# Kernel tuning notes

Measured on AMD Instinct MI355X. Metric: run time of the kernel, lower is better.

## Reference

```python
import jax, jax.numpy as jnp
import numpy as np

N_DOCS = 2_000_000      # shape[0]: number of documents
N_TERMS = 30_000        # vocabulary size (number of CSC columns)
NNZ_PER_COL = 2_000     # posting-list length per term (uniform)
Q = 32                  # active terms in the sparse query
TOP_K = 10


def setup_inputs() -> dict:
    key = jax.random.key(0)
    k1, k2, k3, k4 = jax.random.split(key, 4)
    # Uniform-length CSC column pointers: ccol[t] = t * NNZ_PER_COL
    ccol = jnp.arange(N_TERMS + 1, dtype=jnp.int32) * NNZ_PER_COL
    nnz = N_TERMS * NNZ_PER_COL
    rindices = jax.random.randint(k1, (nnz,), 0, N_DOCS, dtype=jnp.int32)
    cvalues = jax.random.uniform(k2, (nnz,), dtype=jnp.float32)
    indices = jax.random.randint(k3, (1, Q), 0, N_TERMS, dtype=jnp.int32)
    values = jax.random.normal(k4, (1, Q), dtype=jnp.float32)
    return {"ccol": ccol, "rindices": rindices, "cvalues": cvalues,
            "indices": indices, "values": values,
            "n_docs": N_DOCS, "top_k": TOP_K}


def reference(ccol, rindices, cvalues, indices, values, n_docs, top_k):
    idx = indices.reshape(-1)   # [Q] query term ids
    w = values.reshape(-1)      # [Q] query term weights
    # Static max posting-list length (uniform CSC built in setup_inputs).
    L = rindices.shape[0] // (ccol.shape[0] - 1)
    starts = ccol[idx]                       # [Q]
    lens = ccol[idx + 1] - starts            # [Q]
    offs = jnp.arange(L, dtype=starts.dtype) # [L]
    mask = offs[None, :] < lens[:, None]     # [Q, L] valid entries (handles ragged lists)
    pos = jnp.where(mask, starts[:, None] + offs[None, :], 0)  # [Q, L]
    docs = rindices[pos]                                        # [Q, L] doc ids
    contrib = jnp.where(mask, cvalues[pos] * w[:, None], 0.0)   # [Q, L] scaled scores
    # Scatter-add over documents (equivalent to the per-term index_add_ loop).
    accumulated = jnp.zeros((n_docs,), jnp.float32).at[docs.reshape(-1)].add(
        contrib.reshape(-1))
    top_vals, top_idx = jax.lax.top_k(accumulated, top_k)
    return top_vals, top_idx
```

## Files before the change

### kernel.cpp

```cpp
#include <hip/hip_runtime.h>
#include <float.h>
#include <limits.h>


#define TOPK 10
#define BLK  256

__device__ __forceinline__ bool better(float va, int ia, float vb, int ib) {
    return (va > vb) || (va == vb && ia < ib);
}

__device__ __forceinline__ void topk_insert(float (&lv)[TOPK], int (&li)[TOPK],
                                            float v, int i) {
    if (!better(v, i, lv[TOPK - 1], li[TOPK - 1])) return;
#pragma unroll
    for (int k = TOPK - 1; k >= 1; --k) {
        bool ck  = better(v, i, lv[k],     li[k]);
        bool ck1 = better(v, i, lv[k - 1], li[k - 1]);
        float nv = ck ? (ck1 ? lv[k - 1] : v) : lv[k];
        int   ni = ck ? (ck1 ? li[k - 1] : i) : li[k];
        lv[k] = nv; li[k] = ni;
    }
    if (better(v, i, lv[0], li[0])) { lv[0] = v; li[0] = i; }
}

__device__ void block_topk_merge(float (&lv)[TOPK], int (&li)[TOPK],
                                 float* sv, int* si, int tid) {
#pragma unroll
    for (int k = 0; k < TOPK; ++k) { sv[tid * TOPK + k] = lv[k]; si[tid * TOPK + k] = li[k]; }
    for (int off = BLK / 2; off >= 1; off >>= 1) {
        __syncthreads();
        if (tid < off) {
            const int ba = tid * TOPK, bb = (tid + off) * TOPK;
            float mv[TOPK]; int mi[TOPK];
            int a = 0, b = 0;
#pragma unroll
            for (int k = 0; k < TOPK; ++k) {
                float va = sv[ba + a]; int ia = si[ba + a];
                float vb = sv[bb + b]; int ib = si[bb + b];
                bool ta = better(va, ia, vb, ib);
                mv[k] = ta ? va : vb;
                mi[k] = ta ? ia : ib;
                a += ta ? 1 : 0;
                b += ta ? 0 : 1;
            }
#pragma unroll
            for (int k = 0; k < TOPK; ++k) { sv[ba + k] = mv[k]; si[ba + k] = mi[k]; }
        }
    }
    __syncthreads();
}

__global__ void __launch_bounds__(BLK)
zero_touched(const int* __restrict__ ccol, const int* __restrict__ rindices,
             const int* __restrict__ qidx, float* __restrict__ score, int L) {
    const int q = blockIdx.y;
    const int l = blockIdx.x * BLK + threadIdx.x;
    const int term  = qidx[q];
    const int start = ccol[term];
    const int len   = ccol[term + 1] - start;
    if (l < len && l < L) score[rindices[start + l]] = 0.0f;
}

__global__ void __launch_bounds__(BLK)
scatter_add(const int* __restrict__ ccol, const int* __restrict__ rindices,
            const float* __restrict__ cvalues, const int* __restrict__ qidx,
            const float* __restrict__ qval, float* __restrict__ score, int L) {
    const int q = blockIdx.y;
    const int l = blockIdx.x * BLK + threadIdx.x;
    const int term  = qidx[q];
    const int start = ccol[term];
    const int len   = ccol[term + 1] - start;
    if (l < len && l < L) {
        const int pos = start + l;
        atomicAdd(&score[rindices[pos]], cvalues[pos] * qval[q]);
    }
}

__global__ void __launch_bounds__(BLK)
candidates_topk(const int* __restrict__ ccol, const int* __restrict__ rindices,
                const int* __restrict__ qidx, float* __restrict__ score,
                float* __restrict__ cand_v, int* __restrict__ cand_i, int L) {
    __shared__ float sv[BLK * TOPK];
    __shared__ int   si[BLK * TOPK];
    float lv[TOPK]; int li[TOPK];
#pragma unroll
    for (int k = 0; k < TOPK; ++k) { lv[k] = -FLT_MAX; li[k] = INT_MAX; }

    const int q = blockIdx.y;
    const int l = blockIdx.x * BLK + threadIdx.x;
    const int term  = qidx[q];
    const int start = ccol[term];
    const int len   = ccol[term + 1] - start;
    if (l < len && l < L) {
        const int doc = rindices[start + l];
        const float v = atomicExch(&score[doc], -FLT_MAX);
        if (v != -FLT_MAX) topk_insert(lv, li, v, doc);
    }
    block_topk_merge(lv, li, sv, si, threadIdx.x);
    if (threadIdx.x == 0) {
        const int bid = blockIdx.y * gridDim.x + blockIdx.x;
#pragma unroll
        for (int k = 0; k < TOPK; ++k) {
            cand_v[bid * TOPK + k] = sv[k];
            cand_i[bid * TOPK + k] = si[k];
        }
    }
}

__global__ void __launch_bounds__(BLK)
final_topk(const float* __restrict__ cand_v, const int* __restrict__ cand_i,
           int ncand, float* __restrict__ out) {
    __shared__ float sv[BLK * TOPK];
    __shared__ int   si[BLK * TOPK];
    float lv[TOPK]; int li[TOPK];
#pragma unroll
    for (int k = 0; k < TOPK; ++k) { lv[k] = -FLT_MAX; li[k] = INT_MAX; }
    for (int t = threadIdx.x; t < ncand; t += BLK)
        topk_insert(lv, li, cand_v[t], cand_i[t]);
    block_topk_merge(lv, li, sv, si, threadIdx.x);
    if (threadIdx.x == 0) {
#pragma unroll
        for (int k = 0; k < TOPK; ++k) {
            out[k]        = sv[k];
            out[TOPK + k] = (float)si[k];
        }
    }
}

extern "C" void kernel_launch(void* const* d_in, const int* in_sizes, int n_in,
                              void* d_out, int out_size, void* d_ws, size_t ws_size,
                              hipStream_t stream) {
    const int*   ccol     = (const int*)  d_in[0];
    const int*   rindices = (const int*)  d_in[1];
    const float* cvalues  = (const float*)d_in[2];
    const int*   qidx     = (const int*)  d_in[3];
    const float* qval     = (const float*)d_in[4];
    const int n_docs = 2000000;
    const int nterms = in_sizes[0] - 1;
    const int Q      = in_sizes[3];
    const int L      = in_sizes[1] / nterms;

    float* score  = (float*)d_ws;
    char*  p      = (char*)d_ws + (size_t)n_docs * sizeof(float);
    const int lb  = (L + BLK - 1) / BLK;
    const int nblocks = lb * Q;
    float* cand_v = (float*)p;
    int*   cand_i = (int*)(p + (size_t)nblocks * TOPK * sizeof(float));

    dim3 grid(lb, Q);
    zero_touched   <<<grid, BLK, 0, stream>>>(ccol, rindices, qidx, score, L);
    scatter_add    <<<grid, BLK, 0, stream>>>(ccol, rindices, cvalues, qidx, qval, score, L);
    candidates_topk<<<grid, BLK, 0, stream>>>(ccol, rindices, qidx, score, cand_v, cand_i, L);
    final_topk     <<<1,    BLK, 0, stream>>>(cand_v, cand_i, nblocks * TOPK, (float*)d_out);
}
```

Before: 400.5 us.

## Fuse retrieval kernels into one cooperative kernel with grid-wide syncs

Replaces the four launches (zero touched docs, scatter-add, candidate top-k, final top-k) with a single cooperative kernel that separates the phases with grid.sync(). Each thread keeps its doc id and scaled contribution in registers across phases, so posting-list entries are not reloaded. The aim is to remove inter-kernel launch gaps and redundant global loads. In exchange it pays for three grid-wide barriers, needs every block to be resident at once, and adds host-side occupancy and attribute queries, falling back to the old four-kernel path when a cooperative launch is not possible.

```diff
diff --git a/kernel.cpp b/kernel.cpp
--- a/kernel.cpp
+++ b/kernel.cpp
@@ -1,10 +1,13 @@
 #include <hip/hip_runtime.h>
+#include <hip/hip_cooperative_groups.h>
 #include <float.h>
 #include <limits.h>
 
 
 #define TOPK 10
 #define BLK  256
+
+namespace cg = cooperative_groups;
 
 __device__ __forceinline__ bool better(float va, int ia, float vb, int ib) {
     return (va > vb) || (va == vb && ia < ib);
@@ -51,6 +54,71 @@
     __syncthreads();
 }
 
+
+__global__ void __launch_bounds__(BLK, 1)
+fused_retrieval(const int* __restrict__ ccol, const int* __restrict__ rindices,
+                const float* __restrict__ cvalues, const int* __restrict__ qidx,
+                const float* __restrict__ qval, float* __restrict__ score,
+                float* __restrict__ cand_v, int* __restrict__ cand_i,
+                float* __restrict__ out, int L, int lb) {
+    cg::grid_group grid = cg::this_grid();
+    __shared__ float sv[BLK * TOPK];
+    __shared__ int   si[BLK * TOPK];
+
+    const int q     = blockIdx.x / lb;
+    const int l     = (blockIdx.x % lb) * BLK + threadIdx.x;
+    const int term  = qidx[q];
+    const int start = ccol[term];
+    const int len   = ccol[term + 1] - start;
+    const bool active = (l < len) && (l < L);
+
+    int doc = 0; float contrib = 0.0f;
+    if (active) {
+        const int pos = start + l;
+        doc     = rindices[pos];
+        contrib = cvalues[pos] * qval[q];
+        atomicExch(&score[doc], 0.0f);
+    }
+    grid.sync();
+
+    if (active) atomicAdd(&score[doc], contrib);
+    grid.sync();
+
+    float lv[TOPK]; int li[TOPK];
+#pragma unroll
+    for (int k = 0; k < TOPK; ++k) { lv[k] = -FLT_MAX; li[k] = INT_MAX; }
+    if (active) {
+        const float v = atomicExch(&score[doc], -FLT_MAX);
+        if (v != -FLT_MAX) topk_insert(lv, li, v, doc);
+    }
+    block_topk_merge(lv, li, sv, si, threadIdx.x);
+    if (threadIdx.x == 0) {
+#pragma unroll
+        for (int k = 0; k < TOPK; ++k) {
+            cand_v[blockIdx.x * TOPK + k] = sv[k];
+            cand_i[blockIdx.x * TOPK + k] = si[k];
+        }
+    }
+    grid.sync();
+
+    if (blockIdx.x == 0) {
+        const int ncand = gridDim.x * TOPK;
+#pragma unroll
+        for (int k = 0; k < TOPK; ++k) { lv[k] = -FLT_MAX; li[k] = INT_MAX; }
+        for (int t = threadIdx.x; t < ncand; t += BLK)
+            topk_insert(lv, li, cand_v[t], cand_i[t]);
+        block_topk_merge(lv, li, sv, si, threadIdx.x);
+        if (threadIdx.x == 0) {
+#pragma unroll
+            for (int k = 0; k < TOPK; ++k) {
+                out[k]        = sv[k];
+                out[TOPK + k] = (float)si[k];
+            }
+        }
+    }
+}
+
+
 __global__ void __launch_bounds__(BLK)
 zero_touched(const int* __restrict__ ccol, const int* __restrict__ rindices,
              const int* __restrict__ qidx, float* __restrict__ score, int L) {
@@ -86,7 +154,6 @@
     float lv[TOPK]; int li[TOPK];
 #pragma unroll
     for (int k = 0; k < TOPK; ++k) { lv[k] = -FLT_MAX; li[k] = INT_MAX; }
-
     const int q = blockIdx.y;
     const int l = blockIdx.x * BLK + threadIdx.x;
     const int term  = qidx[q];
@@ -139,18 +206,44 @@
     const int n_docs = 2000000;
     const int nterms = in_sizes[0] - 1;
     const int Q      = in_sizes[3];
-    const int L      = in_sizes[1] / nterms;
+    int       L      = in_sizes[1] / nterms;
 
     float* score  = (float*)d_ws;
     char*  p      = (char*)d_ws + (size_t)n_docs * sizeof(float);
-    const int lb  = (L + BLK - 1) / BLK;
+    int    lb     = (L + BLK - 1) / BLK;
     const int nblocks = lb * Q;
     float* cand_v = (float*)p;
     int*   cand_i = (int*)(p + (size_t)nblocks * TOPK * sizeof(float));
-
-    dim3 grid(lb, Q);
-    zero_touched   <<<grid, BLK, 0, stream>>>(ccol, rindices, qidx, score, L);
-    scatter_add    <<<grid, BLK, 0, stream>>>(ccol, rindices, cvalues, qidx, qval, score, L);
-    candidates_topk<<<grid, BLK, 0, stream>>>(ccol, rindices, qidx, score, cand_v, cand_i, L);
-    final_topk     <<<1,    BLK, 0, stream>>>(cand_v, cand_i, nblocks * TOPK, (float*)d_out);
-}
+    float* out    = (float*)d_out;
+
+    bool coop_ok = false;
+    int dev = 0;
+    if (hipGetDevice(&dev) == hipSuccess) {
+        int coop_attr = 0, ncu = 0, maxb = 0;
+        hipDeviceGetAttribute(&coop_attr, hipDeviceAttributeCooperativeLaunch, dev);
+        hipDeviceGetAttribute(&ncu, hipDeviceAttributeMultiprocessorCount, dev);
+        if (coop_attr && ncu > 0 &&
+            hipOccupancyMaxActiveBlocksPerMultiprocessor(&maxb, fused_retrieval,
+                                                         BLK, 0) == hipSuccess &&
+            maxb * ncu >= nblocks) {
+            coop_ok = true;
+        }
+    }
+
+    if (coop_ok) {
+        void* args[] = {(void*)&ccol, (void*)&rindices, (void*)&cvalues, (void*)&qidx,
+                        (void*)&qval, (void*)&score, (void*)&cand_v, (void*)&cand_i,
+                        (void*)&out, (void*)&L, (void*)&lb};
+        if (hipLaunchCooperativeKernel((const void*)fused_retrieval, dim3(nblocks),
+                                       dim3(BLK), args, 0, stream) != hipSuccess)
+            coop_ok = false;
+    }
+
+    if (!coop_ok) {
+        dim3 grid(lb, Q);
+        zero_touched   <<<grid, BLK, 0, stream>>>(ccol, rindices, qidx, score, L);
+        scatter_add    <<<grid, BLK, 0, stream>>>(ccol, rindices, cvalues, qidx, qval, score, L);
+        candidates_topk<<<grid, BLK, 0, stream>>>(ccol, rindices, qidx, score, cand_v, cand_i, L);
+        final_topk     <<<1,    BLK, 0, stream>>>(cand_v, cand_i, nblocks * TOPK, out);
+    }
+}
```

After: 481.1 us. +20.1%, slower.
